# Optimization experiments

Hardware: AMD Instinct MI355X
Metric: run time of the kernel (lower is better)

## Reference

```python
import jax, jax.numpy as jnp
import numpy as np

D = 768
Y_DIM = 3
Z_DIM = 5
LN_EPS = 1e-5
COS_EPS = 1e-8  # F.cosine_similarity eps


def setup_inputs() -> dict:
    key = jax.random.key(0)
    ks = jax.random.split(key, 12)
    B, L = 64, 512
    s = 1.0 / np.sqrt(D)
    return {
        "embeddings": jax.random.normal(ks[0], (B, L, D), jnp.float32),
        "W1": jax.random.normal(ks[1], (D, D), jnp.float32) * s,
        "b1": jnp.zeros((D,), jnp.float32),
        "W2": jax.random.normal(ks[2], (D, D), jnp.float32) * s,
        "b2": jnp.zeros((D,), jnp.float32),
        "gamma": jnp.ones((D,), jnp.float32),
        "beta": jnp.zeros((D,), jnp.float32),
        "Wy": jax.random.normal(ks[3], (D, Y_DIM), jnp.float32) * s,
        "by": jnp.zeros((Y_DIM,), jnp.float32),
        "Wz": jax.random.normal(ks[4], (D, Z_DIM), jnp.float32) * s,
        "bz": jnp.zeros((Z_DIM,), jnp.float32),
    }


def _attention_cal(data):
    # data: [B, L, D]. Original: pairwise cosine similarity [B,L,L], sum over j, /L,
    # anti_sigmoid = 1/(1+exp(x)), softmax over L.
    # Algebraic rewrite: sum_j cos(x_i, x_j) = n_i . (sum_j n_j) with n = x/||x||.
    L = data.shape[1]
    norm = jnp.linalg.norm(data, axis=-1, keepdims=True)
    n = data / jnp.maximum(norm, COS_EPS)              # [B, L, D]
    s = n.sum(axis=1)                                  # [B, D]
    attention_weight = jnp.einsum("bld,bd->bl", n, s) / L  # [B, L]
    anti_sig = 1.0 / (1.0 + jnp.exp(attention_weight))
    return jax.nn.softmax(anti_sig, axis=-1)           # [B, L]


def reference(embeddings, W1, b1, W2, b2, gamma, beta, Wy, by, Wz, bz):
    h1 = embeddings @ W1 + b1
    h2 = jax.nn.relu(h1) @ W2 + b2
    x = embeddings + h2
    mean = x.mean(axis=-1, keepdims=True)
    var = x.var(axis=-1, keepdims=True)
    ff = gamma * (x - mean) * jax.lax.rsqrt(var + LN_EPS) + beta  # [B, L, D]
    out1 = ff @ Wy + by  # [B, L, Y_DIM]
    out2 = ff @ Wz + bz  # [B, L, Z_DIM]
    return (out1, out2, _attention_cal(ff))
```

## Files before the change

kernel.cpp:

```cpp
#include <hip/hip_runtime.h>
#include <hip/hip_bf16.h>
#include <math.h>

#define D_DIM 768
#define B_DIM 64
#define L_DIM 512
#define M_DIM (B_DIM * L_DIM)
#define YD 3
#define ZD 5
#define NCAT 16
#define LN_EPS 1e-5f
#define COS_EPS 1e-8f

typedef short short8v __attribute__((ext_vector_type(8)));
typedef _Float16 half8v __attribute__((ext_vector_type(8)));
typedef float f32x4  __attribute__((ext_vector_type(4)));

__device__ __forceinline__ unsigned short f2bf(float f) {
    unsigned u = __builtin_bit_cast(unsigned, f);
    u = (u + 0x7fffu + ((u >> 16) & 1u)) >> 16;
    return (unsigned short)u;
}
__device__ __forceinline__ float bf2f(unsigned short h) {
    unsigned u = ((unsigned)h) << 16;
    return __builtin_bit_cast(float, u);
}
__device__ __forceinline__ unsigned short f2h(float f) {
    _Float16 h = (_Float16)f;
    return __builtin_bit_cast(unsigned short, h);
}
__device__ __forceinline__ float h2f(unsigned short u) {
    return (float)__builtin_bit_cast(_Float16, u);
}
__device__ __forceinline__ void splith(float v, unsigned short& h, unsigned short& l) {
    h = f2h(v);
    l = f2h(v - h2f(h));
}

__device__ __forceinline__ void gld16(const void* g, void* l) {
    __builtin_amdgcn_global_load_lds(
        (const __attribute__((address_space(1))) void*)g,
        (__attribute__((address_space(3))) void*)l, 16, 0, 0);
}

__global__ __launch_bounds__(256)
void tsplit_kernel(const float* __restrict__ W1, const float* __restrict__ W2,
                   unsigned short* __restrict__ t1h, unsigned short* __restrict__ t1l,
                   unsigned short* __restrict__ t2h, unsigned short* __restrict__ t2l)
{
    const float* W = blockIdx.z ? W2 : W1;
    unsigned short* th = blockIdx.z ? t2h : t1h;
    unsigned short* tl = blockIdx.z ? t2l : t1l;
    __shared__ float t[32][33];
    const int tx = threadIdx.x & 31, ty = threadIdx.x >> 5;
    const int n0 = blockIdx.x * 32, k0 = blockIdx.y * 32;
    #pragma unroll
    for (int j = 0; j < 4; ++j)
        t[ty + 8 * j][tx] = W[(size_t)(k0 + ty + 8 * j) * D_DIM + n0 + tx];
    __syncthreads();
    #pragma unroll
    for (int j = 0; j < 4; ++j) {
        const float v = t[tx][ty + 8 * j];
        unsigned short h, l; splith(v, h, l);
        const size_t o = (size_t)(n0 + ty + 8 * j) * D_DIM + k0 + tx;
        th[o] = h; tl[o] = l;
    }
}

template<int MODE>
__global__ __launch_bounds__(256, 4)
void gemm_mfma(const float* __restrict__ Af,
               const unsigned short* __restrict__ Ah,
               const unsigned short* __restrict__ Bh, const unsigned short* __restrict__ Bl,
               const float* __restrict__ bias, const float* __restrict__ resid,
               unsigned short* __restrict__ out_u16)
{
    __shared__ short8v As[512], Bs_h[512], Bs_l[512];

    const int lin = blockIdx.y * gridDim.x + blockIdx.x;
    const int cpx = (gridDim.x * gridDim.y) >> 3;
    const int lid = (lin & 7) * cpx + (lin >> 3);
    const int bx  = lid % 6;
    const int by  = lid / 6;

    const int tid  = threadIdx.x;
    const int w    = tid >> 6;
    const int lane = tid & 63;
    const int m0   = by * 128;
    const int n0   = bx * 128;
    const int wm   = (w >> 1) * 64;
    const int wn   = (w & 1) * 64;

    const int rr = lane >> 2;
    const int cc = lane & 3;
    const int r0 = w * 32 + rr;
    const int r1 = r0 + 16;
    const int sw0 = (cc ^ ((r0 >> 1) & 3)) * 16;
    const int sw1 = (cc ^ ((r1 >> 1) & 3)) * 16;
    const size_t boff0 = (size_t)(n0 + r0) * 1536 + sw0;
    const size_t boff1 = (size_t)(n0 + r1) * 1536 + sw1;
    const char* pBh = (const char*)Bh; const char* pBl = (const char*)Bl;
    short8v* const dBh0 = Bs_h + w * 128;      short8v* const dBh1 = dBh0 + 64;
    short8v* const dBl0 = Bs_l + w * 128;      short8v* const dBl1 = dBl0 + 64;

    const size_t aoff0 = (size_t)(m0 + r0) * 1536 + sw0;
    const size_t aoff1 = (size_t)(m0 + r1) * 1536 + sw1;
    const char* pAh = (const char*)Ah;
    short8v* const dA0 = As + w * 128;         short8v* const dA1 = dA0 + 64;

    const int ar  = tid >> 1;
    const int ak0 = (tid & 1) * 16;
    const int asw = (ar >> 1) & 3;
    const int sA0 = ar * 4 + (((tid & 1) * 2 + 0) ^ asw);
    const int sA1 = ar * 4 + (((tid & 1) * 2 + 1) ^ asw);
    const float* gA = (MODE == 0) ? (Af + (size_t)(m0 + ar) * D_DIM + ak0) : nullptr;

    const int lc = lane & 15;
    const int lk = lane >> 4;
    int ia[4], ib[4];
    #pragma unroll
    for (int m = 0; m < 4; ++m) { const int r = wm + m * 16 + lc; ia[m] = r * 4 + (lk ^ ((r >> 1) & 3)); }
    #pragma unroll
    for (int n = 0; n < 4; ++n) { const int r = wn + n * 16 + lc; ib[n] = r * 4 + (lk ^ ((r >> 1) & 3)); }

    f32x4 acc[4][4];
    #pragma unroll
    for (int m = 0; m < 4; ++m)
        #pragma unroll
        for (int n = 0; n < 4; ++n) acc[m][n] = (f32x4)(0.f);

    for (int t = 0; t < 24; ++t) {
        const int kk2 = t * 64;
        gld16(pBh + boff0 + kk2, dBh0);
        gld16(pBh + boff1 + kk2, dBh1);
        gld16(pBl + boff0 + kk2, dBl0);
        gld16(pBl + boff1 + kk2, dBl1);
        if (MODE == 0) {
            const int kk = t * 32;
            float tmp[16];
            #pragma unroll
            for (int q = 0; q < 4; ++q) {
                const float4 f = *reinterpret_cast<const float4*>(gA + kk + q * 4);
                tmp[q * 4 + 0] = f.x; tmp[q * 4 + 1] = f.y;
                tmp[q * 4 + 2] = f.z; tmp[q * 4 + 3] = f.w;
            }
            short8v h0, h1;
            #pragma unroll
            for (int e = 0; e < 8; ++e) {
                h0[e] = (short)f2h(tmp[e]);
                h1[e] = (short)f2h(tmp[8 + e]);
            }
            As[sA0] = h0; As[sA1] = h1;
        } else {
            gld16(pAh + aoff0 + kk2, dA0);
            gld16(pAh + aoff1 + kk2, dA1);
        }
        __syncthreads();

        half8v a[4], bh[4], bl[4];
        #pragma unroll
        for (int m = 0; m < 4; ++m) a[m] = __builtin_bit_cast(half8v, As[ia[m]]);
        #pragma unroll
        for (int n = 0; n < 4; ++n) {
            bh[n] = __builtin_bit_cast(half8v, Bs_h[ib[n]]);
            bl[n] = __builtin_bit_cast(half8v, Bs_l[ib[n]]);
        }

        #pragma unroll
        for (int m = 0; m < 4; ++m)
            #pragma unroll
            for (int n = 0; n < 4; ++n) {
                acc[m][n] = __builtin_amdgcn_mfma_f32_16x16x32_f16(a[m], bh[n], acc[m][n], 0, 0, 0);
                acc[m][n] = __builtin_amdgcn_mfma_f32_16x16x32_f16(a[m], bl[n], acc[m][n], 0, 0, 0);
            }
        __syncthreads();
    }

    const int erow = lane >> 4;
    #pragma unroll
    for (int m = 0; m < 4; ++m) {
        #pragma unroll
        for (int n = 0; n < 4; ++n) {
            const int gcol = n0 + wn + n * 16 + lc;
            const float bv = bias[gcol];
            const int grow0 = m0 + wm + m * 16 + erow * 4;
            #pragma unroll
            for (int r = 0; r < 4; ++r) {
                float v = acc[m][n][r] + bv;
                const size_t o = (size_t)(grow0 + r) * D_DIM + gcol;
                if (MODE == 0) {
                    out_u16[o] = f2h(fmaxf(v, 0.f));
                } else {
                    out_u16[o] = f2bf(v + resid[o]);
                }
            }
        }
    }
}

__global__ __launch_bounds__(256)
void ln_kernel(const unsigned short* __restrict__ xfb, const float* __restrict__ gamma,
               const float* __restrict__ beta, unsigned short* __restrict__ ffb,
               float* __restrict__ rnorm)
{
    const int wave = threadIdx.x >> 6;
    const int lane = threadIdx.x & 63;
    const int row  = blockIdx.x * 4 + wave;
    const unsigned short* xr = xfb + (size_t)row * D_DIM;
    unsigned short* fr = ffb + (size_t)row * D_DIM;

    float v[12];
    float sum = 0.f, sumsq = 0.f;
    #pragma unroll
    for (int j = 0; j < 3; ++j) {
        const ushort4 f = *reinterpret_cast<const ushort4*>(&xr[j * 256 + lane * 4]);
        v[j * 4 + 0] = bf2f(f.x); v[j * 4 + 1] = bf2f(f.y);
        v[j * 4 + 2] = bf2f(f.z); v[j * 4 + 3] = bf2f(f.w);
    }
    #pragma unroll
    for (int e = 0; e < 12; ++e) { sum += v[e]; sumsq = fmaf(v[e], v[e], sumsq); }
    #pragma unroll
    for (int m = 1; m < 64; m <<= 1) {
        sum   += __shfl_xor(sum, m);
        sumsq += __shfl_xor(sumsq, m);
    }
    const float mean = sum * (1.f / 768.f);
    const float var  = sumsq * (1.f / 768.f) - mean * mean;
    const float rstd = 1.f / sqrtf(var + LN_EPS);

    float nsq = 0.f;
    #pragma unroll
    for (int j = 0; j < 3; ++j) {
        const int c = j * 256 + lane * 4;
        const float4 g  = *reinterpret_cast<const float4*>(&gamma[c]);
        const float4 bt = *reinterpret_cast<const float4*>(&beta[c]);
        float4 o;
        o.x = fmaf(g.x * (v[j*4+0] - mean), rstd, bt.x);
        o.y = fmaf(g.y * (v[j*4+1] - mean), rstd, bt.y);
        o.z = fmaf(g.z * (v[j*4+2] - mean), rstd, bt.z);
        o.w = fmaf(g.w * (v[j*4+3] - mean), rstd, bt.w);
        nsq = fmaf(o.x, o.x, nsq); nsq = fmaf(o.y, o.y, nsq);
        nsq = fmaf(o.z, o.z, nsq); nsq = fmaf(o.w, o.w, nsq);
        ushort4 ob;
        ob.x = f2bf(o.x); ob.y = f2bf(o.y); ob.z = f2bf(o.z); ob.w = f2bf(o.w);
        *reinterpret_cast<ushort4*>(&fr[c]) = ob;
    }
    #pragma unroll
    for (int m = 1; m < 64; m <<= 1) nsq += __shfl_xor(nsq, m);
    if (lane == 0) rnorm[row] = 1.f / fmaxf(sqrtf(nsq), COS_EPS);
}

__global__ __launch_bounds__(256)
void colsum_kernel(const unsigned short* __restrict__ ffb, const float* __restrict__ rnorm,
                   float* __restrict__ s_part)
{
    const int c = blockIdx.x * 256 + threadIdx.x;
    const int q = blockIdx.y;
    const int b = blockIdx.z;
    const unsigned short* fb = ffb + (size_t)b * L_DIM * D_DIM;
    const float* rb = rnorm + b * L_DIM;
    float acc = 0.f;
    #pragma unroll 4
    for (int l = q * 128; l < q * 128 + 128; ++l)
        acc = fmaf(bf2f(fb[(size_t)l * D_DIM + c]), rb[l], acc);
    s_part[((size_t)b * 4 + q) * D_DIM + c] = acc;
}

__global__ __launch_bounds__(256)
void wcat_kernel(const float* __restrict__ Wy, const float* __restrict__ Wz,
                 const float* __restrict__ s_part, unsigned short* __restrict__ wcat)
{
    const int b = blockIdx.x;
    unsigned short* wb = wcat + (size_t)b * NCAT * D_DIM;
    const float* sp = s_part + (size_t)b * 4 * D_DIM;
    for (int k = threadIdx.x; k < D_DIM; k += 256) {
        #pragma unroll
        for (int y = 0; y < YD; ++y) wb[y * D_DIM + k] = f2bf(Wy[k * YD + y]);
        #pragma unroll
        for (int z = 0; z < ZD; ++z) wb[(YD + z) * D_DIM + k] = f2bf(Wz[k * ZD + z]);
        wb[8 * D_DIM + k] = f2bf(sp[k] + sp[D_DIM + k] + sp[2 * D_DIM + k] + sp[3 * D_DIM + k]);
        #pragma unroll
        for (int n = 9; n < NCAT; ++n) wb[n * D_DIM + k] = 0;
    }
}

__global__ __launch_bounds__(256)
void rowout_mfma(const unsigned short* __restrict__ ffb, const unsigned short* __restrict__ wcat,
                 const float* __restrict__ rnorm,
                 const float* __restrict__ by, const float* __restrict__ bz,
                 float* __restrict__ out1, float* __restrict__ out2,
                 float* __restrict__ aw)
{
    const int w    = threadIdx.x >> 6;
    const int lane = threadIdx.x & 63;
    const int rbase = blockIdx.x * 64 + w * 16;
    const int b     = blockIdx.x >> 3;
    const int idx  = lane & 15;
    const int ak   = (lane >> 4) * 8;

    const unsigned short* arow = ffb + (size_t)(rbase + idx) * D_DIM + ak;
    const unsigned short* brow = wcat + ((size_t)b * NCAT + idx) * D_DIM + ak;

    f32x4 acc = (f32x4)(0.f);
    #pragma unroll 4
    for (int t = 0; t < 24; ++t) {
        const short8v a  = *reinterpret_cast<const short8v*>(arow + t * 32);
        const short8v bb = *reinterpret_cast<const short8v*>(brow + t * 32);
        acc = __builtin_amdgcn_mfma_f32_16x16x32_bf16(a, bb, acc, 0, 0, 0);
    }

    const int erow = lane >> 4;
    #pragma unroll
    for (int r = 0; r < 4; ++r) {
        const int row = rbase + erow * 4 + r;
        const float v = acc[r];
        if (idx < YD) {
            out1[(size_t)row * YD + idx] = v + by[idx];
        } else if (idx < YD + ZD) {
            out2[(size_t)row * ZD + (idx - YD)] = v + bz[idx - YD];
        } else if (idx == 8) {
            const float a_ = v * rnorm[row] * (1.f / (float)L_DIM);
            aw[row] = 1.f / (1.f + expf(a_));
        }
    }
}

__global__ __launch_bounds__(512)
void softmax_kernel(const float* __restrict__ aw, float* __restrict__ attn)
{
    __shared__ float red[8];
    const int b = blockIdx.x;
    const int t = threadIdx.x;
    const int wave = t >> 6, lane = t & 63;
    const float v = aw[b * L_DIM + t];

    float mx = v;
    #pragma unroll
    for (int m = 1; m < 64; m <<= 1) mx = fmaxf(mx, __shfl_xor(mx, m));
    if (lane == 0) red[wave] = mx;
    __syncthreads();
    mx = red[0];
    #pragma unroll
    for (int w = 1; w < 8; ++w) mx = fmaxf(mx, red[w]);
    __syncthreads();

    const float e = expf(v - mx);
    float sm = e;
    #pragma unroll
    for (int m = 1; m < 64; m <<= 1) sm += __shfl_xor(sm, m);
    if (lane == 0) red[wave] = sm;
    __syncthreads();
    float tot = 0.f;
    #pragma unroll
    for (int w = 0; w < 8; ++w) tot += red[w];

    attn[b * L_DIM + t] = e / tot;
}

extern "C" void kernel_launch(void* const* d_in, const int* in_sizes, int n_in,
                              void* d_out, int out_size, void* d_ws, size_t ws_size,
                              hipStream_t stream)
{
    const float* emb   = (const float*)d_in[0];
    const float* W1    = (const float*)d_in[1];
    const float* b1    = (const float*)d_in[2];
    const float* W2    = (const float*)d_in[3];
    const float* b2    = (const float*)d_in[4];
    const float* gamma = (const float*)d_in[5];
    const float* beta  = (const float*)d_in[6];
    const float* Wy    = (const float*)d_in[7];
    const float* by    = (const float*)d_in[8];
    const float* Wz    = (const float*)d_in[9];
    const float* bz    = (const float*)d_in[10];

    float* out = (float*)d_out;
    char*  p   = (char*)d_ws;

    const size_t MD = (size_t)M_DIM * D_DIM;

    unsigned short* h1h   = (unsigned short*)p;  p += MD * 2;
    unsigned short* xfb   = (unsigned short*)p;  p += MD * 2;
    unsigned short* w1t_h = (unsigned short*)p;  p += (size_t)D_DIM * D_DIM * 2;
    unsigned short* w1t_l = (unsigned short*)p;  p += (size_t)D_DIM * D_DIM * 2;
    unsigned short* w2t_h = (unsigned short*)p;  p += (size_t)D_DIM * D_DIM * 2;
    unsigned short* w2t_l = (unsigned short*)p;  p += (size_t)D_DIM * D_DIM * 2;
    float* rnorm  = (float*)p;                   p += (size_t)M_DIM * 4;
    float* awb    = (float*)p;                   p += (size_t)M_DIM * 4;
    float* s_part = (float*)p;                   p += (size_t)B_DIM * 4 * D_DIM * 4;
    unsigned short* wcat = (unsigned short*)p;

    unsigned short* ffb = h1h;

    float* out1 = out;
    float* out2 = out + (size_t)M_DIM * YD;
    float* attn = out + (size_t)M_DIM * (YD + ZD);

    tsplit_kernel<<<dim3(24, 24, 2), 256, 0, stream>>>(W1, W2, w1t_h, w1t_l,
                                                       w2t_h, w2t_l);

    const dim3 gg(D_DIM / 128, M_DIM / 128);
    gemm_mfma<0><<<gg, 256, 0, stream>>>(emb, nullptr, w1t_h, w1t_l,
                                         b1, nullptr, h1h);
    gemm_mfma<1><<<gg, 256, 0, stream>>>(nullptr, h1h, w2t_h, w2t_l,
                                         b2, emb, xfb);

    ln_kernel<<<M_DIM / 4, 256, 0, stream>>>(xfb, gamma, beta, ffb, rnorm);
    colsum_kernel<<<dim3(3, 4, B_DIM), 256, 0, stream>>>(ffb, rnorm, s_part);
    wcat_kernel<<<B_DIM, 256, 0, stream>>>(Wy, Wz, s_part, wcat);
    rowout_mfma<<<M_DIM / 64, 256, 0, stream>>>(ffb, wcat, rnorm, by, bz,
                                                out1, out2, awb);
    softmax_kernel<<<B_DIM, 512, 0, stream>>>(awb, attn);
}
```

Before: 403.8 us.

## Double-buffer LDS tiles in split-fp16 GEMM with explicit vmcnt waits

Converts both GEMM passes to a two-stage LDS ping-pong, where the next K tile's global-to-LDS loads (and, for the first GEMM, the fp32 A prefetch two tiles ahead in registers) are issued before the MFMA work on the current tile. Hand-placed s_waitcnt vmcnt counts and raw barriers replace __syncthreads, so load latency can overlap compute. This doubles LDS use and lowers the occupancy hint from 4 to 3 blocks per CU. The manual wait counts must exactly match the outstanding loads, or the kernel reads stale data.

```diff
diff --git a/kernel.cpp b/kernel.cpp
--- a/kernel.cpp
+++ b/kernel.cpp
@@ -38,7 +38,8 @@
 }
 
 __device__ __forceinline__ void gld16(const void* g, void* l) {
-    __builtin_amdgcn_global_load_lds(
+    __builtin_amdgcn_global_lo\
+ad_lds(
         (const __attribute__((address_space(1))) void*)g,
         (__attribute__((address_space(3))) void*)l, 16, 0, 0);
 }
@@ -67,15 +68,18 @@
     }
 }
 
+#define VMW(N) asm volatile("s_waitcnt vmcnt(" #N ")" ::: "memory")
+#define SBAR() { __builtin_amdgcn_s_barrier(); __builtin_amdgcn_sched_barrier(0); }
+
 template<int MODE>
-__global__ __launch_bounds__(256, 4)
+__global__ __launch_bounds__(256, 3)
 void gemm_mfma(const float* __restrict__ Af,
                const unsigned short* __restrict__ Ah,
                const unsigned short* __restrict__ Bh, const unsigned short* __restrict__ Bl,
                const float* __restrict__ bias, const float* __restrict__ resid,
                unsigned short* __restrict__ out_u16)
 {
-    __shared__ short8v As[512], Bs_h[512], Bs_l[512];
+    __shared__ short8v As[2][512], Bs_h[2][512], Bs_l[2][512];
 
     const int lin = blockIdx.y * gridDim.x + blockIdx.x;
     const int cpx = (gridDim.x * gridDim.y) >> 3;
@@ -97,16 +101,12 @@
     const int r1 = r0 + 16;
     const int sw0 = (cc ^ ((r0 >> 1) & 3)) * 16;
     const int sw1 = (cc ^ ((r1 >> 1) & 3)) * 16;
+    const size_t aoff0 = (size_t)(m0 + r0) * 1536 + sw0;
+    const size_t aoff1 = (size_t)(m0 + r1) * 1536 + sw1;
     const size_t boff0 = (size_t)(n0 + r0) * 1536 + sw0;
     const size_t boff1 = (size_t)(n0 + r1) * 1536 + sw1;
+    const char* pAh = (const char*)Ah;
     const char* pBh = (const char*)Bh; const char* pBl = (const char*)Bl;
-    short8v* const dBh0 = Bs_h + w * 128;      short8v* const dBh1 = dBh0 + 64;
-    short8v* const dBl0 = Bs_l + w * 128;      short8v* const dBl1 = dBl0 + 64;
-
-    const size_t aoff0 = (size_t)(m0 + r0) * 1536 + sw0;
-    const size_t aoff1 = (size_t)(m0 + r1) * 1536 + sw1;
-    const char* pAh = (const char*)Ah;
-    short8v* const dA0 = As + w * 128;         short8v* const dA1 = dA0 + 64;
 
     const int ar  = tid >> 1;
     const int ak0 = (tid & 1) * 16;
@@ -129,51 +129,86 @@
         #pragma unroll
         for (int n = 0; n < 4; ++n) acc[m][n] = (f32x4)(0.f);
 
-    for (int t = 0; t < 24; ++t) {
-        const int kk2 = t * 64;
-        gld16(pBh + boff0 + kk2, dBh0);
-        gld16(pBh + boff1 + kk2, dBh1);
-        gld16(pBl + boff0 + kk2, dBl0);
-        gld16(pBl + boff1 + kk2, dBl1);
-        if (MODE == 0) {
-            const int kk = t * 32;
-            float tmp[16];
-            #pragma unroll
-            for (int q = 0; q < 4; ++q) {
-                const float4 f = *reinterpret_cast<const float4*>(gA + kk + q * 4);
-                tmp[q * 4 + 0] = f.x; tmp[q * 4 + 1] = f.y;
-                tmp[q * 4 + 2] = f.z; tmp[q * 4 + 3] = f.w;
-            }
-            short8v h0, h1;
-            #pragma unroll
-            for (int e = 0; e < 8; ++e) {
-                h0[e] = (short)f2h(tmp[e]);
-                h1[e] = (short)f2h(tmp[8 + e]);
-            }
-            As[sA0] = h0; As[sA1] = h1;
-        } else {
-            gld16(pAh + aoff0 + kk2, dA0);
-            gld16(pAh + aoff1 + kk2, dA1);
+#define ASTAGE(T, B_) \
+    gld16(pAh + aoff0 + (T) * 64, &As[B_][w * 128]); \
+    gld16(pAh + aoff1 + (T) * 64, &As[B_][w * 128 + 64]);
+#define BSTAGE(T, B_) \
+    gld16(pBh + boff0 + (T) * 64, &Bs_h[B_][w * 128]); \
+    gld16(pBh + boff1 + (T) * 64, &Bs_h[B_][w * 128 + 64]); \
+    gld16(pBl + boff0 + (T) * 64, &Bs_l[B_][w * 128]); \
+    gld16(pBl + boff1 + (T) * 64, &Bs_l[B_][w * 128 + 64]);
+#define LOADF(R_, T) { \
+    _Pragma("unroll") \
+    for (int q = 0; q < 4; ++q) { \
+        const float4 f_ = *reinterpret_cast<const float4*>(gA + (T) * 32 + q * 4); \
+        R_[q * 4 + 0] = f_.x; R_[q * 4 + 1] = f_.y; \
+        R_[q * 4 + 2] = f_.z; R_[q * 4 + 3] = f_.w; } }
+#define SPLITW(R_, B_) { \
+    short8v h0_, h1_; \
+    _Pragma("unroll") \
+    for (int e = 0; e < 8; ++e) { \
+        h0_[e] = (short)f2h(R_[e]); \
+        h1_[e] = (short)f2h(R_[8 + e]); } \
+    As[B_][sA0] = h0_; As[B_][sA1] = h1_; }
+#define COMPUTE(B_) { \
+    half8v a_[4], bh_[4], bl_[4]; \
+    _Pragma("unroll") \
+    for (int m = 0; m < 4; ++m) a_[m] = __builtin_bit_cast(half8v, As[B_][ia[m]]); \
+    _Pragma("unroll") \
+    for (int n = 0; n < 4; ++n) { \
+        bh_[n] = __builtin_bit_cast(half8v, Bs_h[B_][ib[n]]); \
+        bl_[n] = __builtin_bit_cast(half8v, Bs_l[B_][ib[n]]); } \
+    _Pragma("unroll") \
+    for (int m = 0; m < 4; ++m) \
+        _Pragma("unroll") \
+        for (int n = 0; n < 4; ++n) { \
+            acc[m][n] = __builtin_amdgcn_mfma_f32_16x16x32_f16(a_[m], bh_[n], acc[m][n], 0, 0, 0); \
+            acc[m][n] = __builtin_amdgcn_mfma_f32_16x16x32_f16(a_[m], bl_[n], acc[m][n], 0, 0, 0); } }
+
+    if (MODE == 0) {
+        float ta[16], tb[16];
+        LOADF(ta, 0);
+        LOADF(tb, 1);
+        BSTAGE(0, 0);
+        SPLITW(ta, 0);
+        asm volatile("s_waitcnt lgkmcnt(0)" ::: "memory");
+        VMW(0);
+        SBAR();
+#define BODY0(T, CUR, NB, RHELD, RLOAD) { \
+        if ((T) + 2 < 24) LOADF(RLOAD, (T) + 2); \
+        if ((T) < 23) { \
+            SPLITW(RHELD, NB); \
+            BSTAGE((T) + 1, NB); \
+            asm volatile("s_waitcnt lgkmcnt(0)" ::: "memory"); \
+        } \
+        if ((T) < 22) { VMW(8); } else if ((T) == 22) { VMW(4); } else { VMW(0); } \
+        SBAR(); \
+        COMPUTE(CUR); \
+        SBAR(); }
+        for (int t2 = 0; t2 < 24; t2 += 2) {
+            BODY0(t2,     0, 1, tb, ta);
+            BODY0(t2 + 1, 1, 0, ta, tb);
         }
-        __syncthreads();
-
-        half8v a[4], bh[4], bl[4];
-        #pragma unroll
-        for (int m = 0; m < 4; ++m) a[m] = __builtin_bit_cast(half8v, As[ia[m]]);
-        #pragma unroll
-        for (int n = 0; n < 4; ++n) {
-            bh[n] = __builtin_bit_cast(half8v, Bs_h[ib[n]]);
-            bl[n] = __builtin_bit_cast(half8v, Bs_l[ib[n]]);
+#undef BODY0
+    } else {
+        ASTAGE(0, 0);
+        BSTAGE(0, 0);
+        VMW(0);
+        SBAR();
+#define BODY1(T, CUR, NB) { \
+        if ((T) < 23) { \
+            ASTAGE((T) + 1, NB); \
+            BSTAGE((T) + 1, NB); \
+            VMW(6); \
+        } else { VMW(0); } \
+        SBAR(); \
+        COMPUTE(CUR); \
+        SBAR(); }
+        for (int t2 = 0; t2 < 24; t2 += 2) {
+            BODY1(t2,     0, 1);
+            BODY1(t2 + 1, 1, 0);
         }
-
-        #pragma unroll
-        for (int m = 0; m < 4; ++m)
-            #pragma unroll
-            for (int n = 0; n < 4; ++n) {
-                acc[m][n] = __builtin_amdgcn_mfma_f32_16x16x32_f16(a[m], bh[n], acc[m][n], 0, 0, 0);
-                acc[m][n] = __builtin_amdgcn_mfma_f32_16x16x32_f16(a[m], bl[n], acc[m][n], 0, 0, 0);
-            }
-        __syncthreads();
+#undef BODY1
     }
 
     const int erow = lane >> 4;
@@ -196,6 +231,11 @@
             }
         }
     }
+#undef ASTAGE
+#undef BSTAGE
+#undef LOADF
+#undef SPLITW
+#undef COMPUTE
 }
 
 __global__ __launch_bounds__(256)
```

Measured after the change: 376.3 us. -6.8%, faster.
